# Performance work log

Hardware: AMD Instinct MI355X
Metric: run time of the kernel (lower is better)

Reference implementation:

```python
import jax, jax.numpy as jnp
import numpy as np

ALPHA = 0.05  # mixprop alpha
GDEP = 2      # propagation depth

B, C_IN, N, T = 2, 16, 4096, 12
C_OUT = 16


def _row_norm_with_self_loop(A):
    # A <- (A + I); A / rowsum(A)
    A = A + jnp.eye(A.shape[0], dtype=A.dtype)
    return A / A.sum(axis=1, keepdims=True)


def _qadj_mul(Ar, Ai, Aj, Ak, x):
    # quaternion Hamilton product of adjacency quaternion (Ar,Ai,Aj,Ak)
    # with feature quaternion (channel dim split into 4 components).
    # x: [b, c, n, t] with c % 4 == 0
    xr, xi, xj, xk = jnp.split(x, 4, axis=1)  # each [b, c/4, n, t]
    mm = lambda A, v: jnp.einsum('vw,bcwt->bcvt', A, v)
    out_r = mm(Ar, xr) - mm(Ai, xi) - mm(Aj, xj) - mm(Ak, xk)
    out_i = mm(Ar, xi) + mm(Ai, xr) + mm(Aj, xk) - mm(Ak, xj)
    out_j = mm(Ar, xj) - mm(Ai, xk) + mm(Aj, xr) + mm(Ak, xi)
    out_k = mm(Ar, xk) + mm(Ai, xj) - mm(Aj, xi) + mm(Ak, xr)
    return jnp.concatenate([out_r, out_i, out_j, out_k], axis=1)


def _make_quaternion_mul(kernel):
    # kernel: [K, c_in//4, c_out] -> hamilton: [K, c_in, c_out]
    r, i, j, k = jnp.split(kernel, 4, axis=2)  # each [K, c_in//4, c_out//4]
    r2 = jnp.concatenate([r, -i, -j, -k], axis=1)
    i2 = jnp.concatenate([i, r, -k, j], axis=1)
    j2 = jnp.concatenate([j, k, r, -i], axis=1)
    k2 = jnp.concatenate([k, -j, i, r], axis=1)
    return jnp.concatenate([r2, i2, j2, k2], axis=2)  # [K, c_in, c_out]


def setup_inputs() -> dict:
    key = jax.random.key(0)
    ks = jax.random.split(key, 6)
    x = jax.random.normal(ks[0], (B, C_IN, N, T), dtype=jnp.float32)
    adp_r = jax.random.uniform(ks[1], (N, N), dtype=jnp.float32)
    adp_i = jax.random.uniform(ks[2], (N, N), dtype=jnp.float32)
    adp_j = jax.random.uniform(ks[3], (N, N), dtype=jnp.float32)
    adp_k = jax.random.uniform(ks[4], (N, N), dtype=jnp.float32)
    weight = jax.random.normal(ks[5], (GDEP + 1, C_IN // 4, C_OUT), dtype=jnp.float32)
    return {"x": x, "adp_r": adp_r, "adp_i": adp_i, "adp_j": adp_j,
            "adp_k": adp_k, "weight": weight}


def reference(x, adp_r, adp_i, adp_j, adp_k, weight):
    a_r = adp_r  # note: r-component is NOT normalized in the original
    a_i = _row_norm_with_self_loop(adp_i)
    a_j = _row_norm_with_self_loop(adp_j)
    a_k = _row_norm_with_self_loop(adp_k)

    h = x
    out = [h]
    for _ in range(GDEP):
        h = ALPHA * x + (1.0 - ALPHA) * _qadj_mul(a_r, a_i, a_j, a_k, h)
        out.append(h)
    xs = jnp.stack(out, axis=2)  # [b, c_in, gdep+1, n, t]

    hamilton = _make_quaternion_mul(weight)  # [gdep+1, c_in, c_out]
    return jnp.einsum('bikht,kij->bjht', xs, hamilton)  # [b, c_out, n, t]
```

## Files before the change

### kernel.cpp

```cpp
#include <hip/hip_runtime.h>

typedef __attribute__((ext_vector_type(8))) short short8;
typedef __attribute__((ext_vector_type(4))) float f32x4;

#define ALPHA_F 0.05f

static __device__ __forceinline__ unsigned short f2bf(float f) {
  unsigned int u = __float_as_uint(f);
  unsigned int r = (u + 0x7fffu + ((u >> 16) & 1u)) >> 16;
  return (unsigned short)r;
}

static __device__ __forceinline__ void gld16(const void* g, void* l) {
  __builtin_amdgcn_global_load_lds((const __attribute__((address_space(1))) void*)g,
                                   (__attribute__((address_space(3))) void*)l, 16, 0, 0);
}

__global__ __launch_bounds__(256) void prep_adj(const float* __restrict__ ar,
    const float* __restrict__ ai, const float* __restrict__ aj, const float* __restrict__ ak,
    unsigned short* __restrict__ Abf)
{
  const int bid = blockIdx.x;
  const int p = bid >> 12;
  const int row = bid & 4095;
  const float* src = (p == 0) ? ar : (p == 1) ? ai : (p == 2) ? aj : ak;
  const float4* r4 = (const float4*)(src + ((size_t)row << 12));
  ushort4* dst = (ushort4*)(Abf + (((size_t)p << 12) + (size_t)row) * 4096);

  if (p == 0) {
    for (int i = threadIdx.x; i < 1024; i += 256) {
      float4 v = r4[i];
      dst[i] = make_ushort4(f2bf(v.x), f2bf(v.y), f2bf(v.z), f2bf(v.w));
    }
  } else {
    float4 vals[4];
    float s = 0.f;
    #pragma unroll
    for (int it = 0; it < 4; ++it) {
      float4 v = r4[threadIdx.x + it * 256];
      vals[it] = v;
      s += v.x + v.y + v.z + v.w;
    }
    #pragma unroll
    for (int off = 32; off >= 1; off >>= 1) s += __shfl_down(s, off, 64);
    __shared__ float red[4];
    if ((threadIdx.x & 63) == 0) red[threadIdx.x >> 6] = s;
    __syncthreads();
    const float inv = 1.0f / (red[0] + red[1] + red[2] + red[3] + 1.0f);
    #pragma unroll
    for (int it = 0; it < 4; ++it) {
      const int i = threadIdx.x + it * 256;
      float4 v = vals[it];
      const int base = i << 2;
      if (row - base >= 0 && row - base < 4) ((float*)&v)[row - base] += 1.0f;
      dst[i] = make_ushort4(f2bf(v.x * inv), f2bf(v.y * inv), f2bf(v.z * inv), f2bf(v.w * inv));
    }
  }
}

__global__ __launch_bounds__(256) void pack_x2(const float* __restrict__ x,
    unsigned short* __restrict__ XT0, float* __restrict__ H1, float* __restrict__ H2)
{
  __shared__ float tile[3072];
  const int nt = blockIdx.x & 15;
  const int c  = (blockIdx.x >> 4) & 15;
  const int b  = blockIdx.x >> 8;
  const int n0 = nt << 8;
  const int col0 = c * 24 + b * 12;
  const size_t base = ((size_t)(b * 16 + c) * 4096 + n0) * 12;
  #pragma unroll
  for (int it = 0; it < 12; ++it) {
    const int idx = it * 256 + threadIdx.x;
    tile[idx] = x[base + idx];
  }
  __syncthreads();
  #pragma unroll
  for (int it = 0; it < 12; ++it) {
    const int idx = it * 256 + threadIdx.x;
    const int t = idx >> 8, i = idx & 255;
    XT0[(size_t)(col0 + t) * 4096 + (n0 + i)] = f2bf(tile[i * 12 + t]);
  }
  #pragma unroll
  for (int it = 0; it < 12; ++it) {
    const int idx = it * 256 + threadIdx.x;
    const int i = idx / 12, t = idx - i * 12;
    const float v = ALPHA_F * tile[i * 12 + t];
    const size_t o = (size_t)(n0 + i) * 384 + (col0 + t);
    H1[o] = v;
    H2[o] = v;
  }
}

#define SBM 64
#define SBN 384
#define SBK 64

__global__ __launch_bounds__(512, 2) void gemm_s(const unsigned short* __restrict__ A,
    const unsigned short* __restrict__ BT, float* __restrict__ H)
{
  __shared__ __align__(16) unsigned short As[2][SBM * SBK];
  __shared__ __align__(16) unsigned short Bs[2][SBN * SBK];
  const int tid = threadIdx.x;
  const int p  = blockIdx.x >> 6;
  const int n0 = (blockIdx.x & 63) << 6;
  const int lane = tid & 63;
  const int w = tid >> 6;
  const int wm = w >> 2;
  const int ws = w & 3;

  f32x4 acc[2][6];
  #pragma unroll
  for (int m = 0; m < 2; ++m)
    #pragma unroll
    for (int n = 0; n < 6; ++n) acc[m][n] = (f32x4){0.f, 0.f, 0.f, 0.f};

  auto stage = [&](int buf, int kt) {
    const int k0 = kt << 6;
    #pragma unroll
    for (int it = 0; it < 7; ++it) {
      const int idx = it * 512 + tid;
      if (it == 0) {
        const int row = idx >> 3, ch = idx & 7;
        const int chs = ch ^ (row & 7);
        gld16(A + (((size_t)(p * 4096 + n0 + row)) << 12) + (size_t)(k0 + chs * 8),
              (unsigned short*)As[buf] + idx * 8);
      } else {
        const int bidx = idx - 512;
        const int row = bidx >> 3, ch = bidx & 7;
        const int chs = ch ^ (row & 7);
        gld16(BT + ((size_t)row << 12) + (size_t)(k0 + chs * 8),
              (unsigned short*)Bs[buf] + bidx * 8);
      }
    }
  };

  stage(0, 0);
  const int l15 = lane & 15, lk = lane >> 4;
  for (int kt = 0; kt < 64; ++kt) {
    const int buf = kt & 1;
    __syncthreads();
    if (kt + 1 < 64) stage(buf ^ 1, kt + 1);
    short8 af[2][2], bf[6][2];
    #pragma unroll
    for (int m = 0; m < 2; ++m) {
      const int row = wm * 32 + m * 16 + l15;
      #pragma unroll
      for (int ks = 0; ks < 2; ++ks) {
        const int ck = (lk + ks * 4) ^ (row & 7);
        af[m][ks] = *(const short8*)&As[buf][row * 64 + ck * 8];
      }
    }
    #pragma unroll
    for (int n = 0; n < 6; ++n) {
      const int row = ws * 96 + n * 16 + l15;
      #pragma unroll
      for (int ks = 0; ks < 2; ++ks) {
        const int ck = (lk + ks * 4) ^ (row & 7);
        bf[n][ks] = *(const short8*)&Bs[buf][row * 64 + ck * 8];
      }
    }
    #pragma unroll
    for (int ks = 0; ks < 2; ++ks)
      #pragma unroll
      for (int m = 0; m < 2; ++m)
        #pragma unroll
        for (int n = 0; n < 6; ++n)
          acc[m][n] = __builtin_amdgcn_mfma_f32_16x16x32_bf16(af[m][ks], bf[n][ks], acc[m][n], 0, 0, 0);
  }

  static const float sgn_t[4][4] = {{1,-1,-1,-1},{1,1,1,-1},{1,-1,1,1},{1,1,-1,1}};
  const int q = ws ^ p;
  const float coef = (1.0f - ALPHA_F) * sgn_t[q][p];
  #pragma unroll
  for (int m = 0; m < 2; ++m) {
    const int nr0 = n0 + wm * 32 + m * 16 + ((lane >> 4) << 2);
    #pragma unroll
    for (int n = 0; n < 6; ++n) {
      const int cc = q * 96 + n * 16 + (lane & 15);
      #pragma unroll
      for (int e = 0; e < 4; ++e)
        atomicAdd(&H[(size_t)(nr0 + e) * 384 + cc], coef * acc[m][n][e]);
    }
  }
}

__global__ __launch_bounds__(256) void pack_h(const float* __restrict__ H,
                                              unsigned short* __restrict__ XT)
{
  __shared__ float T[64][65];
  const int n0 = (blockIdx.x / 6) << 6;
  const int c0 = (blockIdx.x % 6) << 6;
  #pragma unroll
  for (int it = 0; it < 16; ++it) {
    const int idx = it * 256 + threadIdx.x;
    const int r = idx >> 6, cl = idx & 63;
    T[r][cl] = H[(size_t)(n0 + r) * 384 + (c0 + cl)];
  }
  __syncthreads();
  #pragma unroll
  for (int it = 0; it < 16; ++it) {
    const int idx = it * 256 + threadIdx.x;
    const int cc = idx >> 6, rr = idx & 63;
    XT[(size_t)(c0 + cc) * 4096 + (n0 + rr)] = f2bf(T[rr][cc]);
  }
}

__global__ __launch_bounds__(256) void final_k(const float* __restrict__ x,
    const float* __restrict__ H1, const float* __restrict__ H2,
    const float* __restrict__ wgt, float* __restrict__ out)
{
  __shared__ float Hm[3][16][16];
  static const int   comp_t[4][4] = {{0,1,2,3},{1,0,3,2},{2,3,0,1},{3,2,1,0}};
  static const float hsgn_t[4][4] = {{1,-1,-1,-1},{1,1,-1,1},{1,1,1,-1},{1,-1,1,1}};
  for (int idx = threadIdx.x; idx < 768; idx += 256) {
    const int k = idx >> 8, i = (idx >> 4) & 15, j = idx & 15;
    const int J = j >> 2, I = i >> 2, a = i & 3, jj = j & 3;
    Hm[k][i][j] = hsgn_t[J][I] * wgt[(k * 4 + a) * 16 + comp_t[J][I] * 4 + jj];
  }
  __syncthreads();
  const int o = blockIdx.x * 256 + threadIdx.x;
  const int t = o % 12;
  const int nb = o / 12;
  const int n = nb & 4095;
  const int b = nb >> 12;
  float v[3][16];
  #pragma unroll
  for (int i = 0; i < 16; ++i)
    v[0][i] = x[((((size_t)(b * 16 + i)) << 12) | (size_t)n) * 12 + t];
  const int colbase = b * 12 + t;
  #pragma unroll
  for (int i = 0; i < 16; ++i) {
    const size_t hidx = (size_t)n * 384 + (size_t)(i * 24 + colbase);
    v[1][i] = H1[hidx];
    v[2][i] = H2[hidx];
  }
  #pragma unroll
  for (int j = 0; j < 16; ++j) {
    float acc = 0.f;
    #pragma unroll
    for (int k = 0; k < 3; ++k)
      #pragma unroll
      for (int i = 0; i < 16; ++i)
        acc += v[k][i] * Hm[k][i][j];
    out[((((size_t)(b * 16 + j)) << 12) | (size_t)n) * 12 + t] = acc;
  }
}

extern "C" void kernel_launch(void* const* d_in, const int* in_sizes, int n_in,
                              void* d_out, int out_size, void* d_ws, size_t ws_size,
                              hipStream_t stream)
{
  const float* x   = (const float*)d_in[0];
  const float* ar  = (const float*)d_in[1];
  const float* ai  = (const float*)d_in[2];
  const float* aj  = (const float*)d_in[3];
  const float* ak  = (const float*)d_in[4];
  const float* wgt = (const float*)d_in[5];
  float* out = (float*)d_out;

  char* ws = (char*)d_ws;
  unsigned short* Abf = (unsigned short*)(ws);
  unsigned short* XT0 = (unsigned short*)(ws + 134217728);
  unsigned short* XT1 = (unsigned short*)(ws + 137363456);
  float*          H1  = (float*)(ws + 140509184);
  float*          H2  = (float*)(ws + 146800640);

  prep_adj<<<dim3(16384), dim3(256), 0, stream>>>(ar, ai, aj, ak, Abf);
  pack_x2<<<dim3(512), dim3(256), 0, stream>>>(x, XT0, H1, H2);
  gemm_s<<<dim3(256), dim3(512), 0, stream>>>(Abf, XT0, H1);
  pack_h<<<dim3(384), dim3(256), 0, stream>>>(H1, XT1);
  gemm_s<<<dim3(256), dim3(512), 0, stream>>>(Abf, XT1, H2);
  final_k<<<dim3(384), dim3(256), 0, stream>>>(x, H1, H2, wgt, out);
}
```

Baseline: 481.2 us.

## Replace atomic GEMM epilogue with partial buffers and pipeline GEMM k-loop

The GEMM now writes each quaternion-component partial product to its own buffer with plain stores instead of fp32 atomics into a shared H. A new combine kernel applies the signs and alpha mixing with x, then writes H and the transposed bf16 copy for the next hop. The k-loop also replaces __syncthreads with explicit vmcnt waits, raw barriers and MFMA priority raising to overlap loads with compute. This removes atomic contention at the cost of an extra 25 MB partial buffer written and read per hop.

```diff
diff --git a/kernel.cpp b/kernel.cpp
--- a/kernel.cpp
+++ b/kernel.cpp
@@ -58,8 +58,8 @@
   }
 }
 
-__global__ __launch_bounds__(256) void pack_x2(const float* __restrict__ x,
-    unsigned short* __restrict__ XT0, float* __restrict__ H1, float* __restrict__ H2)
+__global__ __launch_bounds__(256) void pack_x(const float* __restrict__ x,
+                                              unsigned short* __restrict__ XT)
 {
   __shared__ float tile[3072];
   const int nt = blockIdx.x & 15;
@@ -78,16 +78,7 @@
   for (int it = 0; it < 12; ++it) {
     const int idx = it * 256 + threadIdx.x;
     const int t = idx >> 8, i = idx & 255;
-    XT0[(size_t)(col0 + t) * 4096 + (n0 + i)] = f2bf(tile[i * 12 + t]);
-  }
-  #pragma unroll
-  for (int it = 0; it < 12; ++it) {
-    const int idx = it * 256 + threadIdx.x;
-    const int i = idx / 12, t = idx - i * 12;
-    const float v = ALPHA_F * tile[i * 12 + t];
-    const size_t o = (size_t)(n0 + i) * 384 + (col0 + t);
-    H1[o] = v;
-    H2[o] = v;
+    XT[(size_t)(col0 + t) * 4096 + (n0 + i)] = f2bf(tile[i * 12 + t]);
   }
 }
 
@@ -95,8 +86,8 @@
 #define SBN 384
 #define SBK 64
 
-__global__ __launch_bounds__(512, 2) void gemm_s(const unsigned short* __restrict__ A,
-    const unsigned short* __restrict__ BT, float* __restrict__ H)
+__global__ __launch_bounds__(512, 2) void gemm_p(const unsigned short* __restrict__ A,
+    const unsigned short* __restrict__ BT, float* __restrict__ P)
 {
   __shared__ __align__(16) unsigned short As[2][SBM * SBK];
   __shared__ __align__(16) unsigned short Bs[2][SBN * SBK];
@@ -136,10 +127,18 @@
 
   stage(0, 0);
   const int l15 = lane & 15, lk = lane >> 4;
-  for (int kt = 0; kt < 64; ++kt) {
+  const int NK = 64;
+  for (int kt = 0; kt < NK; ++kt) {
     const int buf = kt & 1;
-    __syncthreads();
-    if (kt + 1 < 64) stage(buf ^ 1, kt + 1);
+    if (kt + 1 < NK) {
+      stage(buf ^ 1, kt + 1);
+      asm volatile("s_waitcnt vmcnt(7)" ::: "memory");
+    } else {
+      asm volatile("s_waitcnt vmcnt(0)" ::: "memory");
+    }
+    __builtin_amdgcn_s_barrier();
+    __builtin_amdgcn_sched_barrier(0);
+
     short8 af[2][2], bf[6][2];
     #pragma unroll
     for (int m = 0; m < 2; ++m) {
@@ -159,6 +158,7 @@
         bf[n][ks] = *(const short8*)&Bs[buf][row * 64 + ck * 8];
       }
     }
+    __builtin_amdgcn_s_setprio(1);
     #pragma unroll
     for (int ks = 0; ks < 2; ++ks)
       #pragma unroll
@@ -166,42 +166,60 @@
         #pragma unroll
         for (int n = 0; n < 6; ++n)
           acc[m][n] = __builtin_amdgcn_mfma_f32_16x16x32_bf16(af[m][ks], bf[n][ks], acc[m][n], 0, 0, 0);
-  }
-
-  static const float sgn_t[4][4] = {{1,-1,-1,-1},{1,1,1,-1},{1,-1,1,1},{1,1,-1,1}};
-  const int q = ws ^ p;
-  const float coef = (1.0f - ALPHA_F) * sgn_t[q][p];
+    __builtin_amdgcn_s_setprio(0);
+    __builtin_amdgcn_sched_barrier(0);
+    __builtin_amdgcn_s_barrier();
+  }
+
+  float* Pp = P + ((size_t)p * 4096 + (size_t)n0) * 384;
   #pragma unroll
   for (int m = 0; m < 2; ++m) {
-    const int nr0 = n0 + wm * 32 + m * 16 + ((lane >> 4) << 2);
+    const int r0 = wm * 32 + m * 16 + ((lane >> 4) << 2);
     #pragma unroll
     for (int n = 0; n < 6; ++n) {
-      const int cc = q * 96 + n * 16 + (lane & 15);
+      const int cc = ws * 96 + n * 16 + (lane & 15);
       #pragma unroll
       for (int e = 0; e < 4; ++e)
-        atomicAdd(&H[(size_t)(nr0 + e) * 384 + cc], coef * acc[m][n][e]);
-    }
-  }
-}
-
-__global__ __launch_bounds__(256) void pack_h(const float* __restrict__ H,
-                                              unsigned short* __restrict__ XT)
-{
-  __shared__ float T[64][65];
+        Pp[(size_t)(r0 + e) * 384 + cc] = acc[m][n][e];
+    }
+  }
+}
+
+__global__ __launch_bounds__(256) void combine_k(const float* __restrict__ P,
+    const float* __restrict__ x, float* __restrict__ H, unsigned short* __restrict__ XT,
+    const int writeXT)
+{
+  __shared__ unsigned short T[64][72];
   const int n0 = (blockIdx.x / 6) << 6;
   const int c0 = (blockIdx.x % 6) << 6;
-  #pragma unroll
-  for (int it = 0; it < 16; ++it) {
-    const int idx = it * 256 + threadIdx.x;
-    const int r = idx >> 6, cl = idx & 63;
-    T[r][cl] = H[(size_t)(n0 + r) * 384 + (c0 + cl)];
-  }
-  __syncthreads();
-  #pragma unroll
-  for (int it = 0; it < 16; ++it) {
-    const int idx = it * 256 + threadIdx.x;
-    const int cc = idx >> 6, rr = idx & 63;
-    XT[(size_t)(c0 + cc) * 4096 + (n0 + rr)] = f2bf(T[rr][cc]);
+  static const int   sigma_t[4][4] = {{0,1,2,3},{1,0,3,2},{2,3,0,1},{3,2,1,0}};
+  static const float sgn_t[4][4]   = {{1,-1,-1,-1},{1,1,1,-1},{1,-1,1,1},{1,1,-1,1}};
+  #pragma unroll
+  for (int r = 0; r < 16; ++r) {
+    const int idx = r * 256 + threadIdx.x;
+    const int ln = idx >> 6, lc = idx & 63;
+    const int n = n0 + ln, col = c0 + lc;
+    const int q = col / 96;
+    const int cm = col - q * 96;
+    float acc = 0.f;
+    #pragma unroll
+    for (int p = 0; p < 4; ++p)
+      acc += sgn_t[q][p] * P[((size_t)p * 4096 + (size_t)n) * 384 + (size_t)(sigma_t[q][p] * 96 + cm)];
+    const int c = col / 24, rr = col - c * 24;
+    const int b = rr / 12, t = rr - b * 12;
+    const float xv = x[(((size_t)(b * 16 + c) << 12) | (size_t)n) * 12 + t];
+    const float h = ALPHA_F * xv + (1.f - ALPHA_F) * acc;
+    H[(size_t)n * 384 + col] = h;
+    T[lc][ln] = f2bf(h);
+  }
+  if (writeXT) {
+    __syncthreads();
+    #pragma unroll
+    for (int r = 0; r < 16; ++r) {
+      const int idx = r * 256 + threadIdx.x;
+      const int lc = idx >> 6, ln = idx & 63;
+      XT[((size_t)(c0 + lc) << 12) + (size_t)(n0 + ln)] = T[lc][ln];
+    }
   }
 }
 
@@ -262,13 +280,15 @@
   unsigned short* Abf = (unsigned short*)(ws);
   unsigned short* XT0 = (unsigned short*)(ws + 134217728);
   unsigned short* XT1 = (unsigned short*)(ws + 137363456);
-  float*          H1  = (float*)(ws + 140509184);
-  float*          H2  = (float*)(ws + 146800640);
+  float*          P   = (float*)(ws + 140509184);
+  float*          H1  = (float*)(ws + 165675008);
+  float*          H2  = (float*)(ws + 171966464);
 
   prep_adj<<<dim3(16384), dim3(256), 0, stream>>>(ar, ai, aj, ak, Abf);
-  pack_x2<<<dim3(512), dim3(256), 0, stream>>>(x, XT0, H1, H2);
-  gemm_s<<<dim3(256), dim3(512), 0, stream>>>(Abf, XT0, H1);
-  pack_h<<<dim3(384), dim3(256), 0, stream>>>(H1, XT1);
-  gemm_s<<<dim3(256), dim3(512), 0, stream>>>(Abf, XT1, H2);
+  pack_x<<<dim3(512), dim3(256), 0, stream>>>(x, XT0);
+  gemm_p<<<dim3(256), dim3(512), 0, stream>>>(Abf, XT0, P);
+  combine_k<<<dim3(384), dim3(256), 0, stream>>>(P, x, H1, XT1, 1);
+  gemm_p<<<dim3(256), dim3(512), 0, stream>>>(Abf, XT1, P);
+  combine_k<<<dim3(384), dim3(256), 0, stream>>>(P, x, H2, XT1, 0);
   final_k<<<dim3(384), dim3(256), 0, stream>>>(x, H1, H2, wgt, out);
 }
```

Result: slower. 506.9 us (+5.3%).
